# Optimization experiments

Measured on AMD Instinct MI355X. Metric: run time of the kernel, lower is better.

The kernel has to match this reference:

```python
import jax, jax.numpy as jnp
import numpy as np


def setup_inputs() -> dict:
    key = jax.random.key(0)
    k1, k2, k3, k4 = jax.random.split(key, 4)
    bs, c, h, w = 8, 64, 64, 64
    x = jax.random.normal(k1, (bs, c, h, w), dtype=jnp.float32)
    # 1x1 conv weights (bias=False): stored as [out_ch, in_ch]
    wq = jax.random.normal(k2, (c // 2, c), dtype=jnp.float32) * (1.0 / np.sqrt(c))
    wk = jax.random.normal(k3, (c // 2, c), dtype=jnp.float32) * (1.0 / np.sqrt(c))
    wv = jax.random.normal(k4, (c, c), dtype=jnp.float32) * (1.0 / np.sqrt(c))
    return {"x": x, "wq": wq, "wk": wk, "wv": wv}


def reference(x, wq, wk, wv):
    bs, c, h, w = x.shape
    hw = h * w
    xf = x.reshape(bs, c, hw)  # [bs, c, hw]
    # 1x1 convs == per-position matmuls
    q = jnp.einsum('dc,bcn->bnd', wq, xf)   # [bs, hw, c//2]
    k = jnp.einsum('dc,bcn->bdn', wk, xf)   # [bs, c//2, hw]
    v = jnp.einsum('dc,bcn->bdn', wv, xf)   # [bs, c,    hw]
    energy = jnp.einsum('bnd,bdm->bnm', q, k)          # [bs, hw, hw]
    attention = jax.nn.softmax(energy, axis=-1)
    # dropout(p=0.1) is identity in eval mode
    out = jnp.einsum('bcm,bnm->bcn', v, attention)      # [bs, c, hw]
    return out.reshape(bs, c, h, w)
```

## Files before the change

kernel.cpp:

```cpp
#include <hip/hip_runtime.h>
#include <hip/hip_fp16.h>


typedef short          f16x8 __attribute__((ext_vector_type(8)));
typedef float          f32x4 __attribute__((ext_vector_type(4)));
typedef unsigned short u16;
typedef unsigned int   u32;

#define HW  4096
#define CC  64
#define DQK 32
#define NBLK2 256
#define THR2 11.54f

__device__ __forceinline__ u16 f2h(float f) {
    __half h = __float2half(f);
    return *reinterpret_cast<u16*>(&h);
}
__device__ __forceinline__ float h2f(u16 u) {
    __half h; __builtin_memcpy(&h, &u, 2); return __half2float(h);
}
__device__ __forceinline__ u32 pk2(float a, float b) {
    auto r = __builtin_amdgcn_cvt_pkrtz(a, b);
    u32 u; __builtin_memcpy(&u, &r, 4); return u;
}
__device__ __forceinline__ float ex2(float x) {
    return __builtin_amdgcn_exp2f(x);
}
__device__ __forceinline__ float max16(const f32x4* s) {
    float a = fmaxf(fmaxf(s[0][0], s[0][1]), s[0][2]);
    a = fmaxf(fmaxf(a, s[0][3]), s[1][0]);
    a = fmaxf(fmaxf(a, s[1][1]), s[1][2]);
    a = fmaxf(fmaxf(a, s[1][3]), s[2][0]);
    a = fmaxf(fmaxf(a, s[2][1]), s[2][2]);
    a = fmaxf(fmaxf(a, s[2][3]), s[3][0]);
    a = fmaxf(fmaxf(a, s[3][1]), s[3][2]);
    return fmaxf(a, s[3][3]);
}

__global__ __launch_bounds__(256) void proj_kernel(
    const float* __restrict__ x,  const float* __restrict__ wq,
    const float* __restrict__ wk, const float* __restrict__ wv,
    u16* __restrict__ Qr, u16* __restrict__ Kf, u16* __restrict__ Vf)
{
    const int b    = blockIdx.x;
    const int tile = blockIdx.y;
    const int n0   = tile * 64;
    const int tid  = threadIdx.x;

    __shared__ __align__(16) u16 Xt[64][88];

    {
        const int c  = tid >> 2;
        const int nc = (tid & 3) * 16;
        const float* src = x + ((size_t)(b * CC + c) * HW + n0 + nc);
        float fv[16];
        *(f32x4*)(fv)      = *(const f32x4*)(src);
        *(f32x4*)(fv + 4)  = *(const f32x4*)(src + 4);
        *(f32x4*)(fv + 8)  = *(const f32x4*)(src + 8);
        *(f32x4*)(fv + 12) = *(const f32x4*)(src + 12);
        #pragma unroll
        for (int i = 0; i < 16; ++i) Xt[nc + i][c] = f2h(fv[i]);
    }
    __syncthreads();

    const int wave = tid >> 6;
    const int lane = tid & 63;
    const int lr   = lane & 15;
    const int lg   = lane >> 4;
    const int lk   = lg * 8;

    const float* W = (wave == 0) ? wq : (wave == 1) ? wk
                   : (wave == 2) ? wv : (wv + 32 * 64);
    const float scale = (wave == 0) ? 1.4426950408889634f : 1.0f;

    f16x8 a[2][2];
    #pragma unroll
    for (int dt = 0; dt < 2; ++dt)
        #pragma unroll
        for (int h = 0; h < 2; ++h) {
            const float* p = W + (dt * 16 + lr) * 64 + h * 32 + lk;
            f32x4 lo = *(const f32x4*)p, hi = *(const f32x4*)(p + 4);
            u16 t[8];
            #pragma unroll
            for (int j = 0; j < 4; ++j) {
                t[j]     = f2h(lo[j] * scale);
                t[4 + j] = f2h(hi[j] * scale);
            }
            a[dt][h] = *(const f16x8*)t;
        }

    const f32x4 fz = {0.f, 0.f, 0.f, 0.f};
    f32x4 acc[2][4];
    #pragma unroll
    for (int dt = 0; dt < 2; ++dt)
        #pragma unroll
        for (int nt = 0; nt < 4; ++nt) acc[dt][nt] = fz;

    #pragma unroll
    for (int nt = 0; nt < 4; ++nt)
        #pragma unroll
        for (int h = 0; h < 2; ++h) {
            f16x8 bx = *(const f16x8*)(&Xt[nt * 16 + lr][h * 32 + lk]);
            #pragma unroll
            for (int dt = 0; dt < 2; ++dt)
                acc[dt][nt] = __builtin_amdgcn_mfma_f32_16x16x32_f16(
                                  a[dt][h], bx, acc[dt][nt], 0, 0, 0);
        }

    if (wave == 0) {
        #pragma unroll
        for (int dt = 0; dt < 2; ++dt)
            #pragma unroll
            for (int nt = 0; nt < 4; ++nt) {
                const int n = n0 + nt * 16 + lr;
                const int d = dt * 16 + lg * 4;
                u16 pkk[4];
                #pragma unroll
                for (int r = 0; r < 4; ++r) pkk[r] = f2h(acc[dt][nt][r]);
                *(uint2*)(Qr + ((size_t)(b * HW + n) * DQK + d)) = *(uint2*)pkk;
            }
    } else if (wave == 1) {
        #pragma unroll
        for (int dt = 0; dt < 2; ++dt)
            #pragma unroll
            for (int nt = 0; nt < 4; ++nt) {
                const int m_in = nt * 16 + lr;
                const int mt   = 2 * (m_in >> 5) + ((m_in >> 2) & 1);
                const int lrk  = ((m_in >> 4) & 1) * 8 + ((m_in >> 3) & 1) * 4 + (m_in & 3);
                const int lgk  = dt * 2 + (lg >> 1);
                const int j0   = (lg & 1) * 4;
                u16 pkk[4];
                #pragma unroll
                for (int r = 0; r < 4; ++r) pkk[r] = f2h(acc[dt][nt][r]);
                *(uint2*)(Kf + (size_t)(b * 64 + tile) * 2048
                             + mt * 512 + lgk * 128 + lrk * 8 + j0) = *(uint2*)pkk;
            }
    } else {
        const int cbase = (wave - 2) * 32;
        #pragma unroll
        for (int dt = 0; dt < 2; ++dt)
            #pragma unroll
            for (int nt = 0; nt < 4; ++nt) {
                const int m_in = nt * 16 + lr;
                const int h    = m_in >> 5;
                const int lgv  = (m_in >> 3) & 3;
                const int j    = m_in & 7;
                #pragma unroll
                for (int r = 0; r < 4; ++r) {
                    const int c  = cbase + dt * 16 + lg * 4 + r;
                    const int ct = c >> 4, lrv = c & 15;
                    Vf[(size_t)(b * 64 + tile) * 4096
                       + ct * 1024 + h * 512 + lgv * 128 + lrv * 8 + j]
                        = f2h(acc[dt][nt][r]);
                }
            }
    }
}

template<int S>
__global__ __launch_bounds__(256, 4) void attn_kernel(
    const u16* __restrict__ Qr, const u16* __restrict__ Kf,
    const u16* __restrict__ Vf, float* __restrict__ out,
    u16* __restrict__ Opart, float* __restrict__ Ml)
{
    constexpr int NT = HW / S / 64;
    const int b    = blockIdx.x;
    const int nb   = blockIdx.y;
    const int sp   = blockIdx.z;
    const int tid  = threadIdx.x;
    const int wave = tid >> 6;
    const int lane = tid & 63;
    const int lr   = lane & 15;
    const int lg   = lane >> 4;
    const int lk   = lg * 8;

    const int qb = nb * 128 + wave * 32;
    const f16x8 aq0 = *(const f16x8*)(Qr + (size_t)(b * HW + qb + lr) * DQK + lk);
    const f16x8 aq1 = *(const f16x8*)(Qr + (size_t)(b * HW + qb + 16 + lr) * DQK + lk);

    const f16x8 ones = { 0x3C00, 0x3C00, 0x3C00, 0x3C00,
                         0x3C00, 0x3C00, 0x3C00, 0x3C00 };
    const f32x4 fz = {0.f, 0.f, 0.f, 0.f};

    const int tile0 = sp * NT;
    const u16* KfT = Kf + (size_t)(b * 64 + tile0) * 2048 + lg * 128 + lr * 8;
    const u16* VfT = Vf + (size_t)(b * 64 + tile0) * 4096 + lg * 128 + lr * 8;

    f16x8 kf[4], vf[4][2];
    #pragma unroll
    for (int mt = 0; mt < 4; ++mt)
        kf[mt] = *(const f16x8*)(KfT + mt * 512);
    #pragma unroll
    for (int ct = 0; ct < 4; ++ct)
        #pragma unroll
        for (int h = 0; h < 2; ++h)
            vf[ct][h] = *(const f16x8*)(VfT + ct * 1024 + h * 512);

    f32x4 o[2][4];
    #pragma unroll
    for (int qs = 0; qs < 2; ++qs)
        #pragma unroll
        for (int ct = 0; ct < 4; ++ct) o[qs][ct] = fz;
    f32x4 lrow[2] = {fz, fz};
    float mrow[2] = {-1e30f, -1e30f};

    #pragma unroll 2
    for (int t = 0; t < NT; ++t) {
        const int tn = (t + 1 < NT) ? t + 1 : t;

        f32x4 s[4];
        #pragma unroll
        for (int mt = 0; mt < 4; ++mt)
            s[mt] = __builtin_amdgcn_mfma_f32_16x16x32_f16(kf[mt], aq0, fz, 0, 0, 0);

        float lm = max16(s);
        if (__any(lm > mrow[0] + THR2)) {
            float v = lm;
            v = fmaxf(v, __shfl_xor(v, 16, 64));
            v = fmaxf(v, __shfl_xor(v, 32, 64));
            float mnew  = fmaxf(mrow[0], v);
            float alpha = ex2(mrow[0] - mnew);
            mrow[0] = mnew;
            f32x4 al;
            #pragma unroll
            for (int r = 0; r < 4; ++r) al[r] = __shfl(alpha, 4 * lg + r, 64);
            #pragma unroll
            for (int ct = 0; ct < 4; ++ct)
                #pragma unroll
                for (int r = 0; r < 4; ++r) o[0][ct][r] *= al[r];
            #pragma unroll
            for (int r = 0; r < 4; ++r) lrow[0][r] *= al[r];
        }
        f16x8 pa0[2];
        {
            const float m = mrow[0];
            #pragma unroll
            for (int h = 0; h < 2; ++h) {
                u32 w[4];
                w[0] = pk2(ex2(s[2*h][0] - m), ex2(s[2*h][1] - m));
                w[1] = pk2(ex2(s[2*h][2] - m), ex2(s[2*h][3] - m));
                w[2] = pk2(ex2(s[2*h+1][0] - m), ex2(s[2*h+1][1] - m));
                w[3] = pk2(ex2(s[2*h+1][2] - m), ex2(s[2*h+1][3] - m));
                __builtin_memcpy(&pa0[h], w, 16);
            }
        }
        {
            f32x4 rs = __builtin_amdgcn_mfma_f32_16x16x32_f16(pa0[0], ones, fz, 0, 0, 0);
            rs = __builtin_amdgcn_mfma_f32_16x16x32_f16(pa0[1], ones, rs, 0, 0, 0);
            #pragma unroll
            for (int r = 0; r < 4; ++r) lrow[0][r] += rs[r];
        }
        #pragma unroll
        for (int ct = 0; ct < 4; ++ct) {
            o[0][ct] = __builtin_amdgcn_mfma_f32_16x16x32_f16(pa0[0], vf[ct][0], o[0][ct], 0, 0, 0);
            o[0][ct] = __builtin_amdgcn_mfma_f32_16x16x32_f16(pa0[1], vf[ct][1], o[0][ct], 0, 0, 0);
        }

        #pragma unroll
        for (int mt = 0; mt < 4; ++mt)
            s[mt] = __builtin_amdgcn_mfma_f32_16x16x32_f16(kf[mt], aq1, fz, 0, 0, 0);

        #pragma unroll
        for (int mt = 0; mt < 4; ++mt)
            kf[mt] = *(const f16x8*)(KfT + (size_t)tn * 2048 + mt * 512);

        lm = max16(s);
        if (__any(lm > mrow[1] + THR2)) {
            float v = lm;
            v = fmaxf(v, __shfl_xor(v, 16, 64));
            v = fmaxf(v, __shfl_xor(v, 32, 64));
            float mnew  = fmaxf(mrow[1], v);
            float alpha = ex2(mrow[1] - mnew);
            mrow[1] = mnew;
            f32x4 al;
            #pragma unroll
            for (int r = 0; r < 4; ++r) al[r] = __shfl(alpha, 4 * lg + r, 64);
            #pragma unroll
            for (int ct = 0; ct < 4; ++ct)
                #pragma unroll
                for (int r = 0; r < 4; ++r) o[1][ct][r] *= al[r];
            #pragma unroll
            for (int r = 0; r < 4; ++r) lrow[1][r] *= al[r];
        }
        f16x8 pa1[2];
        {
            const float m = mrow[1];
            #pragma unroll
            for (int h = 0; h < 2; ++h) {
                u32 w[4];
                w[0] = pk2(ex2(s[2*h][0] - m), ex2(s[2*h][1] - m));
                w[1] = pk2(ex2(s[2*h][2] - m), ex2(s[2*h][3] - m));
                w[2] = pk2(ex2(s[2*h+1][0] - m), ex2(s[2*h+1][1] - m));
                w[3] = pk2(ex2(s[2*h+1][2] - m), ex2(s[2*h+1][3] - m));
                __builtin_memcpy(&pa1[h], w, 16);
            }
        }
        {
            f32x4 rs = __builtin_amdgcn_mfma_f32_16x16x32_f16(pa1[0], ones, fz, 0, 0, 0);
            rs = __builtin_amdgcn_mfma_f32_16x16x32_f16(pa1[1], ones, rs, 0, 0, 0);
            #pragma unroll
            for (int r = 0; r < 4; ++r) lrow[1][r] += rs[r];
        }
        #pragma unroll
        for (int ct = 0; ct < 4; ++ct) {
            o[1][ct] = __builtin_amdgcn_mfma_f32_16x16x32_f16(pa1[0], vf[ct][0], o[1][ct], 0, 0, 0);
            o[1][ct] = __builtin_amdgcn_mfma_f32_16x16x32_f16(pa1[1], vf[ct][1], o[1][ct], 0, 0, 0);
        }

        #pragma unroll
        for (int ct = 0; ct < 4; ++ct)
            #pragma unroll
            for (int h = 0; h < 2; ++h)
                vf[ct][h] = *(const f16x8*)(VfT + (size_t)tn * 4096 + ct * 1024 + h * 512);
    }

    if constexpr (S == 1) {
        #pragma unroll
        for (int qs = 0; qs < 2; ++qs)
            #pragma unroll
            for (int ct = 0; ct < 4; ++ct) {
                const int c = ct * 16 + lr;
                f32x4 st;
                #pragma unroll
                for (int r = 0; r < 4; ++r) st[r] = o[qs][ct][r] / lrow[qs][r];
                *(f32x4*)(out + (size_t)(b * CC + c) * HW + qb + qs * 16 + lg * 4) = st;
            }
    } else {
        const int bnb = b * 32 + nb;
        u16* Op = Opart + ((size_t)(sp * NBLK2 + bnb) * 64) * 128;
        #pragma unroll
        for (int qs = 0; qs < 2; ++qs)
            #pragma unroll
            for (int ct = 0; ct < 4; ++ct) {
                const int c    = ct * 16 + lr;
                const int qloc = wave * 32 + qs * 16 + lg * 4;
                u16 pkk[4];
                #pragma unroll
                for (int r = 0; r < 4; ++r) pkk[r] = f2h(o[qs][ct][r] / lrow[qs][r]);
                *(uint2*)(Op + (size_t)c * 128 + qloc) = *(uint2*)pkk;
            }
        float* Mp = Ml + (size_t)(sp * NBLK2 + bnb) * 256;
        if (lg == 0) {
            Mp[wave * 32 + lr]      = mrow[0];
            Mp[wave * 32 + 16 + lr] = mrow[1];
        }
        if (lr == 0) {
            #pragma unroll
            for (int qs = 0; qs < 2; ++qs)
                #pragma unroll
                for (int r = 0; r < 4; ++r)
                    Mp[128 + wave * 32 + qs * 16 + 4 * lg + r] = lrow[qs][r];
        }
    }
}

template<int S>
__global__ __launch_bounds__(256) void combine_kernel(
    const u16* __restrict__ Opart, const float* __restrict__ Ml,
    float* __restrict__ out)
{
    const int bnb = blockIdx.x;
    const int b = bnb >> 5, nb = bnb & 31;
    const int tid = threadIdx.x;
    const int c  = tid >> 2;
    const int q0 = (tid & 3) * 32;

    #pragma unroll
    for (int qq = 0; qq < 32; qq += 4) {
        const int q = q0 + qq;
        f32x4 wl[S];
        f32x4 den = {0.f, 0.f, 0.f, 0.f};
        f32x4 M;
        {
            f32x4 ms[S], ls[S];
            #pragma unroll
            for (int s = 0; s < S; ++s) {
                const float* Mp = Ml + (size_t)(s * NBLK2 + bnb) * 256;
                ms[s] = *(const f32x4*)(Mp + q);
                ls[s] = *(const f32x4*)(Mp + 128 + q);
            }
            M = ms[0];
            #pragma unroll
            for (int s = 1; s < S; ++s)
                #pragma unroll
                for (int j = 0; j < 4; ++j) M[j] = fmaxf(M[j], ms[s][j]);
            #pragma unroll
            for (int s = 0; s < S; ++s)
                #pragma unroll
                for (int j = 0; j < 4; ++j) {
                    wl[s][j] = ex2(ms[s][j] - M[j]) * ls[s][j];
                    den[j] += wl[s][j];
                }
        }
        f32x4 acc = {0.f, 0.f, 0.f, 0.f};
        #pragma unroll
        for (int s = 0; s < S; ++s) {
            uint2 hv = *(const uint2*)(Opart +
                          ((size_t)(s * NBLK2 + bnb) * 64 + c) * 128 + q);
            u16 h4[4]; __builtin_memcpy(h4, &hv, 8);
            #pragma unroll
            for (int j = 0; j < 4; ++j) acc[j] += wl[s][j] * h2f(h4[j]);
        }
        #pragma unroll
        for (int j = 0; j < 4; ++j) acc[j] /= den[j];
        *(f32x4*)(out + (size_t)(b * CC + c) * HW + nb * 128 + q) = acc;
    }
}

extern "C" void kernel_launch(void* const* d_in, const int* in_sizes, int n_in,
                              void* d_out, int out_size, void* d_ws, size_t ws_size,
                              hipStream_t stream)
{
    const float* x  = (const float*)d_in[0];
    const float* wq = (const float*)d_in[1];
    const float* wk = (const float*)d_in[2];
    const float* wv = (const float*)d_in[3];
    u16* ws  = (u16*)d_ws;
    u16* Qr  = ws;
    u16* Kf  = ws + (size_t)8 * HW * DQK;
    u16* Vf  = ws + (size_t)16 * HW * DQK;
    u16* Opart = ws + (size_t)4194304;
    float* out = (float*)d_out;

    proj_kernel<<<dim3(8, 64), 256, 0, stream>>>(x, wq, wk, wv, Qr, Kf, Vf);

    const size_t qkv_b   = 8ull * 1024 * 1024;
    const size_t opart_b = (size_t)NBLK2 * 64 * 128 * 2;
    const size_t ml_b    = (size_t)NBLK2 * 256 * 4;

    if (ws_size >= qkv_b + 4 * (opart_b + ml_b)) {
        float* Ml = (float*)(Opart + 4ull * NBLK2 * 64 * 128);
        attn_kernel<4><<<dim3(8, 32, 4), 256, 0, stream>>>(Qr, Kf, Vf, out, Opart, Ml);
        combine_kernel<4><<<NBLK2, 256, 0, stream>>>(Opart, Ml, out);
    } else if (ws_size >= qkv_b + 2 * (opart_b + ml_b)) {
        float* Ml = (float*)(Opart + 2ull * NBLK2 * 64 * 128);
        attn_kernel<2><<<dim3(8, 32, 2), 256, 0, stream>>>(Qr, Kf, Vf, out, Opart, Ml);
        combine_kernel<2><<<NBLK2, 256, 0, stream>>>(Opart, Ml, out);
    } else {
        attn_kernel<1><<<dim3(8, 32, 1), 256, 0, stream>>>(Qr, Kf, Vf, out, nullptr, nullptr);
    }
}
```

Baseline: 67.47 us.

## Add 8-way key split, vectorize V stores, fold row-sum into MFMA accumulator

Adds an 8-way split of the key dimension for the attention kernel, which runs when the workspace is large enough, doubling grid parallelism at the cost of more partial outputs for the combine step. The projection kernel swaps MFMA operands for V so that its fp16 output can be written with packed 8-byte stores instead of scattered 2-byte stores. The softmax row-sum MFMA now accumulates directly into lrow, dropping the separate add. The combine kernel is restructured to stream the per-split max and sum values, which reduces register arrays when S is larger.

Result: slower. 79.86 us (+18.4%).

```diff
diff --git a/kernel.cpp b/kernel.cpp
--- a/kernel.cpp
+++ b/kernel.cpp
@@ -97,63 +97,74 @@
         #pragma unroll
         for (int nt = 0; nt < 4; ++nt) acc[dt][nt] = fz;
 
-    #pragma unroll
-    for (int nt = 0; nt < 4; ++nt)
-        #pragma unroll
-        for (int h = 0; h < 2; ++h) {
-            f16x8 bx = *(const f16x8*)(&Xt[nt * 16 + lr][h * 32 + lk]);
+    if (wave < 2) {
+        #pragma unroll
+        for (int nt = 0; nt < 4; ++nt)
+            #pragma unroll
+            for (int h = 0; h < 2; ++h) {
+                f16x8 bx = *(const f16x8*)(&Xt[nt * 16 + lr][h * 32 + lk]);
+                #pragma unroll
+                for (int dt = 0; dt < 2; ++dt)
+                    acc[dt][nt] = __builtin_amdgcn_mfma_f32_16x16x32_f16(
+                                      a[dt][h], bx, acc[dt][nt], 0, 0, 0);
+            }
+        if (wave == 0) {
             #pragma unroll
             for (int dt = 0; dt < 2; ++dt)
-                acc[dt][nt] = __builtin_amdgcn_mfma_f32_16x16x32_f16(
-                                  a[dt][h], bx, acc[dt][nt], 0, 0, 0);
-        }
-
-    if (wave == 0) {
+                #pragma unroll
+                for (int nt = 0; nt < 4; ++nt) {
+                    const int n = n0 + nt * 16 + lr;
+                    const int d = dt * 16 + lg * 4;
+                    u16 pkk[4];
+                    #pragma unroll
+                    for (int r = 0; r < 4; ++r) pkk[r] = f2h(acc[dt][nt][r]);
+                    *(uint2*)(Qr + ((size_t)(b * HW + n) * DQK + d)) = *(uint2*)pkk;
+                }
+        } else {
+            #pragma unroll
+            for (int dt = 0; dt < 2; ++dt)
+                #pragma unroll
+                for (int nt = 0; nt < 4; ++nt) {
+                    const int m_in = nt * 16 + lr;
+                    const int mt   = 2 * (m_in >> 5) + ((m_in >> 2) & 1);
+                    const int lrk  = ((m_in >> 4) & 1) * 8 + ((m_in >> 3) & 1) * 4 + (m_in & 3);
+                    const int lgk  = dt * 2 + (lg >> 1);
+                    const int j0   = (lg & 1) * 4;
+                    u16 pkk[4];
+                    #pragma unroll
+                    for (int r = 0; r < 4; ++r) pkk[r] = f2h(acc[dt][nt][r]);
+                    *(uint2*)(Kf + (size_t)(b * 64 + tile) * 2048
+                                 + mt * 512 + lgk * 128 + lrk * 8 + j0) = *(uint2*)pkk;
+                }
+        }
+    } else {
+        #pragma unroll
+        for (int nt = 0; nt < 4; ++nt)
+            #pragma unroll
+            for (int h = 0; h < 2; ++h) {
+                f16x8 bx = *(const f16x8*)(&Xt[nt * 16 + lr][h * 32 + lk]);
+                #pragma unroll
+                for (int dt = 0; dt < 2; ++dt)
+                    acc[dt][nt] = __builtin_amdgcn_mfma_f32_16x16x32_f16(
+                                      bx, a[dt][h], acc[dt][nt], 0, 0, 0);
+            }
+        const int cbase = (wave - 2) * 32;
         #pragma unroll
         for (int dt = 0; dt < 2; ++dt)
             #pragma unroll
             for (int nt = 0; nt < 4; ++nt) {
-                const int n = n0 + nt * 16 + lr;
-                const int d = dt * 16 + lg * 4;
+                const int c   = cbase + dt * 16 + lr;
+                const int ct  = c >> 4, lrv = c & 15;
+                const int m0  = nt * 16 + 4 * lg;
+                const int h   = m0 >> 5;
+                const int lgv = (m0 >> 3) & 3;
+                const int j0  = m0 & 7;
                 u16 pkk[4];
                 #pragma unroll
                 for (int r = 0; r < 4; ++r) pkk[r] = f2h(acc[dt][nt][r]);
-                *(uint2*)(Qr + ((size_t)(b * HW + n) * DQK + d)) = *(uint2*)pkk;
-            }
-    } else if (wave == 1) {
-        #pragma unroll
-        for (int dt = 0; dt < 2; ++dt)
-            #pragma unroll
-            for (int nt = 0; nt < 4; ++nt) {
-                const int m_in = nt * 16 + lr;
-                const int mt   = 2 * (m_in >> 5) + ((m_in >> 2) & 1);
-                const int lrk  = ((m_in >> 4) & 1) * 8 + ((m_in >> 3) & 1) * 4 + (m_in & 3);
-                const int lgk  = dt * 2 + (lg >> 1);
-                const int j0   = (lg & 1) * 4;
-                u16 pkk[4];
-                #pragma unroll
-                for (int r = 0; r < 4; ++r) pkk[r] = f2h(acc[dt][nt][r]);
-                *(uint2*)(Kf + (size_t)(b * 64 + tile) * 2048
-                             + mt * 512 + lgk * 128 + lrk * 8 + j0) = *(uint2*)pkk;
-            }
-    } else {
-        const int cbase = (wave - 2) * 32;
-        #pragma unroll
-        for (int dt = 0; dt < 2; ++dt)
-            #pragma unroll
-            for (int nt = 0; nt < 4; ++nt) {
-                const int m_in = nt * 16 + lr;
-                const int h    = m_in >> 5;
-                const int lgv  = (m_in >> 3) & 3;
-                const int j    = m_in & 7;
-                #pragma unroll
-                for (int r = 0; r < 4; ++r) {
-                    const int c  = cbase + dt * 16 + lg * 4 + r;
-                    const int ct = c >> 4, lrv = c & 15;
-                    Vf[(size_t)(b * 64 + tile) * 4096
-                       + ct * 1024 + h * 512 + lgv * 128 + lrv * 8 + j]
-                        = f2h(acc[dt][nt][r]);
-                }
+                *(uint2*)(Vf + (size_t)(b * 64 + tile) * 4096
+                             + ct * 1024 + h * 512 + lgv * 128 + lrv * 8 + j0)
+                    = *(uint2*)pkk;
             }
     }
 }
@@ -245,12 +256,8 @@
                 __builtin_memcpy(&pa0[h], w, 16);
             }
         }
-        {
-            f32x4 rs = __builtin_amdgcn_mfma_f32_16x16x32_f16(pa0[0], ones, fz, 0, 0, 0);
-            rs = __builtin_amdgcn_mfma_f32_16x16x32_f16(pa0[1], ones, rs, 0, 0, 0);
-            #pragma unroll
-            for (int r = 0; r < 4; ++r) lrow[0][r] += rs[r];
-        }
+        lrow[0] = __builtin_amdgcn_mfma_f32_16x16x32_f16(pa0[0], ones, lrow[0], 0, 0, 0);
+        lrow[0] = __builtin_amdgcn_mfma_f32_16x16x32_f16(pa0[1], ones, lrow[0], 0, 0, 0);
         #pragma unroll
         for (int ct = 0; ct < 4; ++ct) {
             o[0][ct] = __builtin_amdgcn_mfma_f32_16x16x32_f16(pa0[0], vf[ct][0], o[0][ct], 0, 0, 0);
@@ -296,12 +303,8 @@
                 __builtin_memcpy(&pa1[h], w, 16);
             }
         }
-        {
-            f32x4 rs = __builtin_amdgcn_mfma_f32_16x16x32_f16(pa1[0], ones, fz, 0, 0, 0);
-            rs = __builtin_amdgcn_mfma_f32_16x16x32_f16(pa1[1], ones, rs, 0, 0, 0);
-            #pragma unroll
-            for (int r = 0; r < 4; ++r) lrow[1][r] += rs[r];
-        }
+        lrow[1] = __builtin_amdgcn_mfma_f32_16x16x32_f16(pa1[0], ones, lrow[1], 0, 0, 0);
+        lrow[1] = __builtin_amdgcn_mfma_f32_16x16x32_f16(pa1[1], ones, lrow[1], 0, 0, 0);
         #pragma unroll
         for (int ct = 0; ct < 4; ++ct) {
             o[1][ct] = __builtin_amdgcn_mfma_f32_16x16x32_f16(pa1[0], vf[ct][0], o[1][ct], 0, 0, 0);
@@ -369,38 +372,30 @@
     #pragma unroll
     for (int qq = 0; qq < 32; qq += 4) {
         const int q = q0 + qq;
-        f32x4 wl[S];
+        f32x4 M = {-1e30f, -1e30f, -1e30f, -1e30f};
+        #pragma unroll
+        for (int s = 0; s < S; ++s) {
+            const float* Mp = Ml + (size_t)(s * NBLK2 + bnb) * 256;
+            f32x4 ms = *(const f32x4*)(Mp + q);
+            #pragma unroll
+            for (int j = 0; j < 4; ++j) M[j] = fmaxf(M[j], ms[j]);
+        }
         f32x4 den = {0.f, 0.f, 0.f, 0.f};
-        f32x4 M;
-        {
-            f32x4 ms[S], ls[S];
-            #pragma unroll
-            for (int s = 0; s < S; ++s) {
-                const float* Mp = Ml + (size_t)(s * NBLK2 + bnb) * 256;
-                ms[s] = *(const f32x4*)(Mp + q);
-                ls[s] = *(const f32x4*)(Mp + 128 + q);
-            }
-            M = ms[0];
-            #pragma unroll
-            for (int s = 1; s < S; ++s)
-                #pragma unroll
-                for (int j = 0; j < 4; ++j) M[j] = fmaxf(M[j], ms[s][j]);
-            #pragma unroll
-            for (int s = 0; s < S; ++s)
-                #pragma unroll
-                for (int j = 0; j < 4; ++j) {
-                    wl[s][j] = ex2(ms[s][j] - M[j]) * ls[s][j];
-                    den[j] += wl[s][j];
-                }
-        }
         f32x4 acc = {0.f, 0.f, 0.f, 0.f};
         #pragma unroll
         for (int s = 0; s < S; ++s) {
+            const float* Mp = Ml + (size_t)(s * NBLK2 + bnb) * 256;
+            f32x4 ms = *(const f32x4*)(Mp + q);
+            f32x4 ls = *(const f32x4*)(Mp + 128 + q);
             uint2 hv = *(const uint2*)(Opart +
                           ((size_t)(s * NBLK2 + bnb) * 64 + c) * 128 + q);
             u16 h4[4]; __builtin_memcpy(h4, &hv, 8);
             #pragma unroll
-            for (int j = 0; j < 4; ++j) acc[j] += wl[s][j] * h2f(h4[j]);
+            for (int j = 0; j < 4; ++j) {
+                float w = ex2(ms[j] - M[j]) * ls[j];
+                den[j] += w;
+                acc[j] += w * h2f(h4[j]);
+            }
         }
         #pragma unroll
         for (int j = 0; j < 4; ++j) acc[j] /= den[j];
@@ -429,7 +424,11 @@
     const size_t opart_b = (size_t)NBLK2 * 64 * 128 * 2;
     const size_t ml_b    = (size_t)NBLK2 * 256 * 4;
 
-    if (ws_size >= qkv_b + 4 * (opart_b + ml_b)) {
+    if (ws_size >= qkv_b + 8 * (opart_b + ml_b)) {
+        float* Ml = (float*)(Opart + 8ull * NBLK2 * 64 * 128);
+        attn_kernel<8><<<dim3(8, 32, 8), 256, 0, stream>>>(Qr, Kf, Vf, out, Opart, Ml);
+        combine_kernel<8><<<NBLK2, 256, 0, stream>>>(Opart, Ml, out);
+    } else if (ws_size >= qkv_b + 4 * (opart_b + ml_b)) {
         float* Ml = (float*)(Opart + 4ull * NBLK2 * 64 * 128);
         attn_kernel<4><<<dim3(8, 32, 4), 256, 0, stream>>>(Qr, Kf, Vf, out, Opart, Ml);
         combine_kernel<4><<<NBLK2, 256, 0, stream>>>(Opart, Ml, out);
```
